# Kernel tuning notes

Hardware: AMD Instinct MI355X
Metric: run time of the kernel (lower is better)

The kernel has to match this reference:

```python
import jax, jax.numpy as jnp
import numpy as np

NUM_HEADS = 12
D_MODEL = 768
D_K = D_MODEL // NUM_HEADS


def setup_inputs() -> dict:
    key = jax.random.key(0)
    k0, k1, k2, k3, k4 = jax.random.split(key, 5)
    B, S = 4, 2048
    scale = 1.0 / np.sqrt(D_MODEL)
    return {
        "x": jax.random.normal(k0, (B, S, D_MODEL), dtype=jnp.float32),
        "wq": jax.random.normal(k1, (D_MODEL, D_MODEL), dtype=jnp.float32) * scale,
        "wk": jax.random.normal(k2, (D_MODEL, D_MODEL), dtype=jnp.float32) * scale,
        "wv": jax.random.normal(k3, (D_MODEL, D_MODEL), dtype=jnp.float32) * scale,
        "wo": jax.random.normal(k4, (D_MODEL, D_MODEL), dtype=jnp.float32) * scale,
    }


def reference(x, wq, wk, wv, wo):
    # x: [B, S, d_model]; weights are torch Linear weights [out, in], applied as x @ W^T
    B, S, _ = x.shape
    q = (x @ wq.T).reshape(B, S, NUM_HEADS, D_K).transpose(0, 2, 1, 3)  # [B,H,S,dk]
    k = (x @ wk.T).reshape(B, S, NUM_HEADS, D_K).transpose(0, 2, 1, 3)
    v = (x @ wv.T).reshape(B, S, NUM_HEADS, D_K).transpose(0, 2, 1, 3)
    # Note: original calls scaled_dot_product_attention(queries, keys, values),
    # whose body computes (first_arg @ second_arg^T) => standard Q K^T scores.
    scores = jnp.einsum("bhqd,bhkd->bhqk", q, k) / jnp.sqrt(jnp.float32(D_K))
    causal_mask = jnp.triu(jnp.ones((S, S), dtype=bool), k=1)  # True above diagonal
    scores = jnp.where(causal_mask, -jnp.inf, scores)
    probs = jax.nn.softmax(scores, axis=-1)  # stable max-subtracted softmax, as in source
    attn = jnp.einsum("bhqk,bhkd->bhqd", probs, v)  # [B,H,S,dk]
    attn = attn.transpose(0, 2, 1, 3).reshape(B, S, D_MODEL)
    return attn @ wo.T
```

## Files before the change

### kernel.cpp

```cpp
#include <hip/hip_runtime.h>
#include <stdint.h>

#define DMODEL 768
#define NHEADS 12
#define DK 64
#define BATCH 4
#define SEQ 2048
#define MTOK (BATCH*SEQ)

typedef float f32x4 __attribute__((ext_vector_type(4)));
typedef float f32x16 __attribute__((ext_vector_type(16)));
typedef short bf16x8 __attribute__((ext_vector_type(8)));
typedef unsigned short u16;
typedef unsigned int u32;

#define LOG2E 1.4426950408889634f

__device__ __forceinline__ u16 f2bf(float f) {
  uint32_t u = __float_as_uint(f);
  u += 0x7FFFu + ((u >> 16) & 1u);
  return (u16)(u >> 16);
}

#define GLDS16(g, l) __builtin_amdgcn_global_load_lds( \
    (const __attribute__((address_space(1))) unsigned int*)(g), \
    (__attribute__((address_space(3))) unsigned int*)(l), 16, 0, 0)

__global__ void cvt_kernel(const float* __restrict__ src, u16* __restrict__ dst, int n4) {
  int i = blockIdx.x * blockDim.x + threadIdx.x;
  if (i >= n4) return;
  float4 v = reinterpret_cast<const float4*>(src)[i];
  ushort4 o;
  o.x = f2bf(v.x); o.y = f2bf(v.y); o.z = f2bf(v.z); o.w = f2bf(v.w);
  reinterpret_cast<ushort4*>(dst)[i] = o;
}

__global__ void cvt_w4(const float* __restrict__ w0, const float* __restrict__ w1,
                       const float* __restrict__ w2, const float* __restrict__ w3,
                       u16* __restrict__ dst, int n4) {
  int i = blockIdx.x * blockDim.x + threadIdx.x;
  if (i >= n4) return;
  const float* src = (blockIdx.y == 0) ? w0 : (blockIdx.y == 1) ? w1 : (blockIdx.y == 2) ? w2 : w3;
  float4 v = reinterpret_cast<const float4*>(src)[i];
  ushort4 o;
  o.x = f2bf(v.x); o.y = f2bf(v.y); o.z = f2bf(v.z); o.w = f2bf(v.w);
  reinterpret_cast<ushort4*>(dst + (size_t)blockIdx.y * DMODEL * DMODEL)[i] = o;
}

#define BM 128
#define BN 128
#define BK 32

__device__ __forceinline__ void gemm_loop(const u16* __restrict__ A, const u16* __restrict__ W,
                                          int bm, int bn, int t, u16* As, u16* Ws,
                                          f32x4 (&acc)[4][4]) {
  const int lane = t & 63;
  const int wave = t >> 6;
  const int r16 = lane & 15, g = lane >> 4;
  const int wr = (wave >> 1) * 64;
  const int wc = (wave & 1) * 64;
  const int c0 = t, c1 = t + 256;
  const int r0 = c0 >> 2, k0 = ((c0 & 3) ^ ((c0 >> 3) & 3)) * 8;
  const int r1 = c1 >> 2, k1 = ((c1 & 3) ^ ((c1 >> 3) & 3)) * 8;
  const size_t a0 = (size_t)(bm + r0) * DMODEL + k0;
  const size_t a1 = (size_t)(bm + r1) * DMODEL + k1;
  const size_t w0 = (size_t)(bn + r0) * DMODEL + k0;
  const size_t w1 = (size_t)(bn + r1) * DMODEL + k1;

  GLDS16(A + a0, As + c0 * 8); GLDS16(A + a1, As + c1 * 8);
  GLDS16(W + w0, Ws + c0 * 8); GLDS16(W + w1, Ws + c1 * 8);
  __syncthreads();

  const int NK = DMODEL / BK;
  for (int kt = 0; kt < NK; ++kt) {
    const int cur = kt & 1;
    if (kt + 1 < NK) {
      const size_t koff = (size_t)(kt + 1) * BK;
      GLDS16(A + a0 + koff, As + (cur ^ 1) * 4096 + c0 * 8);
      GLDS16(A + a1 + koff, As + (cur ^ 1) * 4096 + c1 * 8);
      GLDS16(W + w0 + koff, Ws + (cur ^ 1) * 4096 + c0 * 8);
      GLDS16(W + w1 + koff, Ws + (cur ^ 1) * 4096 + c1 * 8);
    }
    bf16x8 af[4], bfr[4];
#pragma unroll
    for (int m = 0; m < 4; ++m) {
      const int row = wr + m * 16 + r16;
      af[m] = *reinterpret_cast<const bf16x8*>(&As[cur * 4096 + row * 32 + ((g ^ ((row >> 1) & 3)) * 8)]);
    }
#pragma unroll
    for (int n = 0; n < 4; ++n) {
      const int row = wc + n * 16 + r16;
      bfr[n] = *reinterpret_cast<const bf16x8*>(&Ws[cur * 4096 + row * 32 + ((g ^ ((row >> 1) & 3)) * 8)]);
    }
#pragma unroll
    for (int m = 0; m < 4; ++m)
#pragma unroll
      for (int n = 0; n < 4; ++n)
        acc[m][n] = __builtin_amdgcn_mfma_f32_16x16x32_bf16(af[m], bfr[n], acc[m][n], 0, 0, 0);
    __syncthreads();
  }
}

__launch_bounds__(256)
__global__ void qkv_gemm(const u16* __restrict__ A, const u16* __restrict__ wAll,
                         u16* __restrict__ Qw, u16* __restrict__ Kw, u16* __restrict__ Vtw) {
  __shared__ __align__(16) u16 As[2 * BM * BK];
  __shared__ __align__(16) u16 Ws[2 * BN * BK];
  const int t = threadIdx.x;
  const int lane = t & 63, wave = t >> 6;
  const int r16 = lane & 15, g = lane >> 4;
  const int bm = blockIdx.x * BM, bn = blockIdx.y * BN;
  const int z = blockIdx.z;
  const u16* W = wAll + (size_t)z * DMODEL * DMODEL;
  const int wr = (wave >> 1) * 64, wc = (wave & 1) * 64;

  f32x4 acc[4][4] = {};
  gemm_loop(A, W, bm, bn, t, As, Ws, acc);

  if (z <= 1) {
    u16* Qo = (z == 0) ? Qw : Kw;
    const float scl = (z == 0) ? (0.125f * LOG2E) : 1.0f;
#pragma unroll
    for (int m = 0; m < 4; ++m) {
      const int gi0 = bm + wr + m * 16 + g * 4;
#pragma unroll
      for (int n = 0; n < 4; ++n) {
        const int gj = bn + wc + n * 16 + r16;
        const int h = gj >> 6, dc = gj & 63;
#pragma unroll
        for (int r = 0; r < 4; ++r) {
          const int gi = gi0 + r;
          const int b_ = gi >> 11, s = gi & 2047;
          Qo[((size_t)((b_ * NHEADS + h) * SEQ + s) << 6) + dc] = f2bf(acc[m][n][r] * scl);
        }
      }
    }
  } else {
#pragma unroll
    for (int m = 0; m < 4; ++m) {
      const int gi0 = bm + wr + m * 16 + g * 4;
      const int b_ = gi0 >> 11, s0 = gi0 & 2047;
#pragma unroll
      for (int n = 0; n < 4; ++n) {
        const int gj = bn + wc + n * 16 + r16;
        const int h = gj >> 6, dc = gj & 63;
        ushort4 pk;
        pk.x = f2bf(acc[m][n][0]); pk.y = f2bf(acc[m][n][1]);
        pk.z = f2bf(acc[m][n][2]); pk.w = f2bf(acc[m][n][3]);
        *reinterpret_cast<ushort4*>(Vtw + ((size_t)((b_ * NHEADS + h) * DK + dc) * SEQ + s0)) = pk;
      }
    }
  }
}

__launch_bounds__(256)
__global__ void out_gemm(const u16* __restrict__ A, const u16* __restrict__ W,
                         float* __restrict__ C) {
  __shared__ __align__(16) u16 As[2 * BM * BK];
  __shared__ __align__(16) u16 Ws[2 * BN * BK];
  const int t = threadIdx.x;
  const int lane = t & 63, wave = t >> 6;
  const int r16 = lane & 15, g = lane >> 4;
  const int bm = blockIdx.x * BM, bn = blockIdx.y * BN;
  const int wr = (wave >> 1) * 64, wc = (wave & 1) * 64;

  f32x4 acc[4][4] = {};
  gemm_loop(A, W, bm, bn, t, As, Ws, acc);

#pragma unroll
  for (int m = 0; m < 4; ++m) {
    const int gi0 = bm + wr + m * 16 + g * 4;
#pragma unroll
    for (int n = 0; n < 4; ++n) {
      const int gj = bn + wc + n * 16 + r16;
#pragma unroll
      for (int r = 0; r < 4; ++r)
        C[(size_t)(gi0 + r) * DMODEL + gj] = acc[m][n][r];
    }
  }
}

__device__ __forceinline__ bf16x8 mk_pa(int hi, float p0, float p1, float p2, float p3,
                                        float p4, float p5, float p6, float p7) {
  u32 w01, w23, w45, w67;
  asm("v_cvt_pk_bf16_f32 %0, %1, %2" : "=v"(w01) : "v"(p0), "v"(p1));
  asm("v_cvt_pk_bf16_f32 %0, %1, %2" : "=v"(w23) : "v"(p2), "v"(p3));
  asm("v_cvt_pk_bf16_f32 %0, %1, %2" : "=v"(w45) : "v"(p4), "v"(p5));
  asm("v_cvt_pk_bf16_f32 %0, %1, %2" : "=v"(w67) : "v"(p6), "v"(p7));
  const u32 pw01 = (u32)__shfl_xor((int)w01, 32);
  const u32 pw23 = (u32)__shfl_xor((int)w23, 32);
  const u32 pw45 = (u32)__shfl_xor((int)w45, 32);
  const u32 pw67 = (u32)__shfl_xor((int)w67, 32);
  union { u32 w[4]; bf16x8 v; } u;
  u.w[0] = hi ? pw45 : w01;
  u.w[1] = hi ? pw67 : w23;
  u.w[2] = hi ? w45  : pw01;
  u.w[3] = hi ? w67  : pw23;
  return u.v;
}

__launch_bounds__(256, 2)
__global__ void attn_kernel(const u16* __restrict__ Qg, const u16* __restrict__ Kg,
                            const u16* __restrict__ Vtg, u16* __restrict__ Og) {
  __shared__ __align__(16) u16 Ks[2][64 * 64];
  __shared__ __align__(16) u16 Vs[2][64 * 64];
  const int t = threadIdx.x;
  const int lane = t & 63, warp = t >> 6;
  const int l31 = lane & 31, hi = lane >> 5;
  const int bx = blockIdx.x;
  const int qt = 15 - (bx / 48);
  const int hb = bx % 48;
  const int h = hb % NHEADS, b = hb / NHEADS;
  const int q0w = qt * 128 + warp * 32;
  const int nt = 2 * qt + 2;
  const size_t bh = (size_t)(b * NHEADS + h);
  const u16* Qb = Qg + bh * SEQ * DK;
  const u16* Kb = Kg + bh * SEQ * DK;
  const u16* Vb = Vtg + bh * DK * SEQ;

  int srow[2], scol[2];
#pragma unroll
  for (int j = 0; j < 2; ++j) {
    const int bb = (t + j * 256) * 16;
    srow[j] = bb >> 7;
    scol[j] = ((bb & 127) ^ ((srow[j] & 7) << 4)) >> 1;
  }

  const int q = q0w + l31;
  bf16x8 qf[4];
#pragma unroll
  for (int kk = 0; kk < 4; ++kk)
    qf[kk] = *reinterpret_cast<const bf16x8*>(Qb + (size_t)q * DK + kk * 16 + hi * 8);

  f32x16 o0 = {}, o1 = {};
  float m = -__builtin_inff(), l = 0.f;
  const int hi4 = hi * 4;
  const int xr = (l31 & 7) << 4;

#pragma unroll
  for (int j = 0; j < 2; ++j) {
    GLDS16(Kb + (size_t)srow[j] * DK + scol[j], &Ks[0][0] + (t + j * 256) * 8);
    GLDS16(Vb + (size_t)srow[j] * SEQ + scol[j], &Vs[0][0] + (t + j * 256) * 8);
  }
  __syncthreads();

  for (int i = 0; i < nt; ++i) {
    const int cur = i & 1;
    const int kv0 = i * 64;
    if (i + 1 < nt) {
      const int nkv0 = kv0 + 64;
#pragma unroll
      for (int j = 0; j < 2; ++j) {
        GLDS16(Kb + (size_t)(nkv0 + srow[j]) * DK + scol[j], &Ks[cur ^ 1][0] + (t + j * 256) * 8);
        GLDS16(Vb + (size_t)srow[j] * SEQ + nkv0 + scol[j], &Vs[cur ^ 1][0] + (t + j * 256) * 8);
      }
    }

    if (kv0 <= q0w + 31) {
      f32x16 t0 = {}, t1 = {};
      const char* Kc = (const char*)Ks[cur];
      __builtin_amdgcn_s_setprio(1);
#pragma unroll
      for (int kk = 0; kk < 4; ++kk) {
        const int cb = kk * 32 + hi * 16;
        bf16x8 a0 = *reinterpret_cast<const bf16x8*>(Kc + ((l31 * 128 + cb) ^ xr));
        bf16x8 a1 = *reinterpret_cast<const bf16x8*>(Kc + (((l31 + 32) * 128 + cb) ^ xr));
        t0 = __builtin_amdgcn_mfma_f32_32x32x16_bf16(a0, qf[kk], t0, 0, 0, 0);
        t1 = __builtin_amdgcn_mfma_f32_32x32x16_bf16(a1, qf[kk], t1, 0, 0, 0);
      }
      __builtin_amdgcn_s_setprio(0);

      if (kv0 + 63 > q0w) {
        const int qmh = (q - kv0) - hi4;
#pragma unroll
        for (int r = 0; r < 16; ++r) {
          const int kvc = (r & 3) + 8 * (r >> 2);
          if (kvc > qmh)      t0[r] = -__builtin_inff();
          if (kvc + 32 > qmh) t1[r] = -__builtin_inff();
        }
      }

      float x0 = fmaxf(t0[0], t0[1]),  x1 = fmaxf(t0[2], t0[3]);
      float x2 = fmaxf(t0[4], t0[5]),  x3 = fmaxf(t0[6], t0[7]);
      float x4 = fmaxf(t0[8], t0[9]),  x5 = fmaxf(t0[10], t0[11]);
      float x6 = fmaxf(t0[12], t0[13]), x7 = fmaxf(t0[14], t0[15]);
      x0 = fmaxf(x0, x1); x2 = fmaxf(x2, x3); x4 = fmaxf(x4, x5); x6 = fmaxf(x6, x7);
      float y0 = fmaxf(t1[0], t1[1]),  y1 = fmaxf(t1[2], t1[3]);
      float y2 = fmaxf(t1[4], t1[5]),  y3 = fmaxf(t1[6], t1[7]);
      float y4 = fmaxf(t1[8], t1[9]),  y5 = fmaxf(t1[10], t1[11]);
      float y6 = fmaxf(t1[12], t1[13]), y7 = fmaxf(t1[14], t1[15]);
      y0 = fmaxf(y0, y1); y2 = fmaxf(y2, y3); y4 = fmaxf(y4, y5); y6 = fmaxf(y6, y7);
      float pm = fmaxf(fmaxf(fmaxf(x0, x2), fmaxf(x4, x6)),
                       fmaxf(fmaxf(y0, y2), fmaxf(y4, y6)));
      pm = fmaxf(pm, __shfl_xor(pm, 32));

      if (pm > m) {
        const float corr = __builtin_amdgcn_exp2f(m - pm);
        l *= corr;
        o0 = o0 * corr;
        o1 = o1 * corr;
        m = pm;
      }

#pragma unroll
      for (int r = 0; r < 16; ++r) { t0[r] = __builtin_amdgcn_exp2f(t0[r] - m); }
#pragma unroll
      for (int r = 0; r < 16; ++r) { t1[r] = __builtin_amdgcn_exp2f(t1[r] - m); }
      float s0 = 0.f, s1 = 0.f, s2 = 0.f, s3 = 0.f;
#pragma unroll
      for (int r = 0; r < 4; ++r) {
        s0 += t0[r]; s1 += t0[4 + r]; s2 += t0[8 + r]; s3 += t0[12 + r];
        s0 += t1[r]; s1 += t1[4 + r]; s2 += t1[8 + r]; s3 += t1[12 + r];
      }
      float s = (s0 + s1) + (s2 + s3);
      l += s + __shfl_xor(s, 32);

      bf16x8 pa0 = mk_pa(hi, t0[0], t0[1], t0[2], t0[3], t0[4], t0[5], t0[6], t0[7]);
      bf16x8 pa1 = mk_pa(hi, t0[8], t0[9], t0[10], t0[11], t0[12], t0[13], t0[14], t0[15]);
      bf16x8 pa2 = mk_pa(hi, t1[0], t1[1], t1[2], t1[3], t1[4], t1[5], t1[6], t1[7]);
      bf16x8 pa3 = mk_pa(hi, t1[8], t1[9], t1[10], t1[11], t1[12], t1[13], t1[14], t1[15]);

      const char* Vc = (const char*)Vs[cur];
      __builtin_amdgcn_s_setprio(1);
#pragma unroll
      for (int ks = 0; ks < 4; ++ks) {
        const int cb = ks * 32 + hi * 16;
        bf16x8 v0 = *reinterpret_cast<const bf16x8*>(Vc + ((l31 * 128 + cb) ^ xr));
        bf16x8 v1 = *reinterpret_cast<const bf16x8*>(Vc + (((l31 + 32) * 128 + cb) ^ xr));
        const bf16x8 pk = (ks == 0) ? pa0 : (ks == 1) ? pa1 : (ks == 2) ? pa2 : pa3;
        o0 = __builtin_amdgcn_mfma_f32_32x32x16_bf16(v0, pk, o0, 0, 0, 0);
        o1 = __builtin_amdgcn_mfma_f32_32x32x16_bf16(v1, pk, o1, 0, 0, 0);
      }
      __builtin_amdgcn_s_setprio(0);
    }
    __syncthreads();
  }

  const float rinv = 1.0f / l;
  u16* orow = Og + (size_t)(b * SEQ + q) * DMODEL + h * 64;
#pragma unroll
  for (int j = 0; j < 4; ++j) {
    ushort4 pk;
    pk.x = f2bf(o0[4 * j + 0] * rinv); pk.y = f2bf(o0[4 * j + 1] * rinv);
    pk.z = f2bf(o0[4 * j + 2] * rinv); pk.w = f2bf(o0[4 * j + 3] * rinv);
    *reinterpret_cast<ushort4*>(orow + 8 * j + hi4) = pk;
  }
#pragma unroll
  for (int j = 0; j < 4; ++j) {
    ushort4 pk;
    pk.x = f2bf(o1[4 * j + 0] * rinv); pk.y = f2bf(o1[4 * j + 1] * rinv);
    pk.z = f2bf(o1[4 * j + 2] * rinv); pk.w = f2bf(o1[4 * j + 3] * rinv);
    *reinterpret_cast<ushort4*>(orow + 32 + 8 * j + hi4) = pk;
  }
}

extern "C" void kernel_launch(void* const* d_in, const int* in_sizes, int n_in,
                              void* d_out, int out_size, void* d_ws, size_t ws_size,
                              hipStream_t stream) {
  const float* x  = (const float*)d_in[0];
  const float* wq = (const float*)d_in[1];
  const float* wk = (const float*)d_in[2];
  const float* wv = (const float*)d_in[3];
  const float* wo = (const float*)d_in[4];

  const size_t SZ_TOK = (size_t)MTOK * DMODEL * 2;
  const size_t SZ_W   = (size_t)DMODEL * DMODEL * 2;
  char* ws = (char*)d_ws;
  size_t off = 0;
  u16* xb  = (u16*)(ws + off); off += SZ_TOK;
  u16* wqb = (u16*)(ws + off); off += 4 * SZ_W;
  u16* Qw  = (u16*)(ws + off); off += SZ_TOK;
  u16* Kw  = (u16*)(ws + off); off += SZ_TOK;
  u16* Vtw = (u16*)(ws + off); off += SZ_TOK;
  u16* Ow  = (u16*)(ws + off); off += SZ_TOK;
  if (ws_size < off) return;
  u16* wob = wqb + 3 * (size_t)DMODEL * DMODEL;

  const int nx4 = MTOK * DMODEL / 4;
  const int nw4 = DMODEL * DMODEL / 4;
  cvt_kernel<<<nx4 / 256, 256, 0, stream>>>(x, xb, nx4);
  cvt_w4<<<dim3(nw4 / 256, 4), 256, 0, stream>>>(wq, wk, wv, wo, wqb, nw4);

  qkv_gemm<<<dim3(MTOK / BM, DMODEL / BN, 3), 256, 0, stream>>>(xb, wqb, Qw, Kw, Vtw);

  attn_kernel<<<dim3(768), 256, 0, stream>>>(Qw, Kw, Vtw, Ow);

  out_gemm<<<dim3(MTOK / BM, DMODEL / BN), 256, 0, stream>>>(Ow, wob, (float*)d_out);
}
```

Measured before the change: 211.3 us.

## Merge conversion kernels, halve attention and out-GEMM tiles for more blocks

```diff
diff --git a/kernel.cpp b/kernel.cpp
--- a/kernel.cpp
+++ b/kernel.cpp
@@ -26,25 +26,27 @@
     (const __attribute__((address_space(1))) unsigned int*)(g), \
     (__attribute__((address_space(3))) unsigned int*)(l), 16, 0, 0)
 
-__global__ void cvt_kernel(const float* __restrict__ src, u16* __restrict__ dst, int n4) {
+__global__ void cvt_all(const float* __restrict__ x,
+                        const float* __restrict__ wq, const float* __restrict__ wk,
+                        const float* __restrict__ wv, const float* __restrict__ wo,
+                        u16* __restrict__ xb, u16* __restrict__ wb) {
+  const int NX = MTOK * DMODEL / 4;
+  const int NW = DMODEL * DMODEL / 4;
   int i = blockIdx.x * blockDim.x + threadIdx.x;
-  if (i >= n4) return;
-  float4 v = reinterpret_cast<const float4*>(src)[i];
+  const float* src; u16* dst; int idx;
+  if (i < NX) {
+    src = x; dst = xb; idx = i;
+  } else {
+    const int j = i - NX;
+    const int w = j / NW;
+    idx = j - w * NW;
+    src = (w == 0) ? wq : (w == 1) ? wk : (w == 2) ? wv : wo;
+    dst = wb + (size_t)w * DMODEL * DMODEL;
+  }
+  float4 v = reinterpret_cast<const float4*>(src)[idx];
   ushort4 o;
   o.x = f2bf(v.x); o.y = f2bf(v.y); o.z = f2bf(v.z); o.w = f2bf(v.w);
-  reinterpret_cast<ushort4*>(dst)[i] = o;
-}
-
-__global__ void cvt_w4(const float* __restrict__ w0, const float* __restrict__ w1,
-                       const float* __restrict__ w2, const float* __restrict__ w3,
-                       u16* __restrict__ dst, int n4) {
-  int i = blockIdx.x * blockDim.x + threadIdx.x;
-  if (i >= n4) return;
-  const float* src = (blockIdx.y == 0) ? w0 : (blockIdx.y == 1) ? w1 : (blockIdx.y == 2) ? w2 : w3;
-  float4 v = reinterpret_cast<const float4*>(src)[i];
-  ushort4 o;
-  o.x = f2bf(v.x); o.y = f2bf(v.y); o.z = f2bf(v.z); o.w = f2bf(v.w);
-  reinterpret_cast<ushort4*>(dst + (size_t)blockIdx.y * DMODEL * DMODEL)[i] = o;
+  reinterpret_cast<ushort4*>(dst)[idx] = o;
 }
 
 #define BM 128
@@ -156,19 +158,56 @@
 __launch_bounds__(256)
 __global__ void out_gemm(const u16* __restrict__ A, const u16* __restrict__ W,
                          float* __restrict__ C) {
-  __shared__ __align__(16) u16 As[2 * BM * BK];
+  __shared__ __align__(16) u16 As[2 * 64 * BK];
   __shared__ __align__(16) u16 Ws[2 * BN * BK];
   const int t = threadIdx.x;
   const int lane = t & 63, wave = t >> 6;
   const int r16 = lane & 15, g = lane >> 4;
-  const int bm = blockIdx.x * BM, bn = blockIdx.y * BN;
-  const int wr = (wave >> 1) * 64, wc = (wave & 1) * 64;
-
-  f32x4 acc[4][4] = {};
-  gemm_loop(A, W, bm, bn, t, As, Ws, acc);
-
-#pragma unroll
-  for (int m = 0; m < 4; ++m) {
+  const int bm = blockIdx.x * 64, bn = blockIdx.y * BN;
+  const int wr = (wave >> 1) * 32, wc = (wave & 1) * 64;
+
+  const int ca = t, ra = ca >> 2, ka = ((ca & 3) ^ ((ca >> 3) & 3)) * 8;
+  const int c1 = t + 256, r1 = c1 >> 2, k1 = ((c1 & 3) ^ ((c1 >> 3) & 3)) * 8;
+  const size_t aoff = (size_t)(bm + ra) * DMODEL + ka;
+  const size_t w0 = (size_t)(bn + ra) * DMODEL + ka;
+  const size_t w1 = (size_t)(bn + r1) * DMODEL + k1;
+
+  f32x4 acc[2][4] = {};
+
+  GLDS16(A + aoff, As + ca * 8);
+  GLDS16(W + w0, Ws + ca * 8); GLDS16(W + w1, Ws + c1 * 8);
+  __syncthreads();
+
+  const int NK = DMODEL / BK;
+  for (int kt = 0; kt < NK; ++kt) {
+    const int cur = kt & 1;
+    if (kt + 1 < NK) {
+      const size_t koff = (size_t)(kt + 1) * BK;
+      GLDS16(A + aoff + koff, As + (cur ^ 1) * 2048 + ca * 8);
+      GLDS16(W + w0 + koff, Ws + (cur ^ 1) * 4096 + ca * 8);
+      GLDS16(W + w1 + koff, Ws + (cur ^ 1) * 4096 + c1 * 8);
+    }
+    bf16x8 af[2], bfr[4];
+#pragma unroll
+    for (int m = 0; m < 2; ++m) {
+      const int row = wr + m * 16 + r16;
+      af[m] = *reinterpret_cast<const bf16x8*>(&As[cur * 2048 + row * 32 + ((g ^ ((row >> 1) & 3)) * 8)]);
+    }
+#pragma unroll
+    for (int n = 0; n < 4; ++n) {
+      const int row = wc + n * 16 + r16;
+      bfr[n] = *reinterpret_cast<const bf16x8*>(&Ws[cur * 4096 + row * 32 + ((g ^ ((row >> 1) & 3)) * 8)]);
+    }
+#pragma unroll
+    for (int m = 0; m < 2; ++m)
+#pragma unroll
+      for (int n = 0; n < 4; ++n)
+        acc[m][n] = __builtin_amdgcn_mfma_f32_16x16x32_bf16(af[m], bfr[n], acc[m][n], 0, 0, 0);
+    __syncthreads();
+  }
+
+#pragma unroll
+  for (int m = 0; m < 2; ++m) {
     const int gi0 = bm + wr + m * 16 + g * 4;
 #pragma unroll
     for (int n = 0; n < 4; ++n) {
@@ -199,7 +238,7 @@
   return u.v;
 }
 
-__launch_bounds__(256, 2)
+__launch_bounds__(128)
 __global__ void attn_kernel(const u16* __restrict__ Qg, const u16* __restrict__ Kg,
                             const u16* __restrict__ Vtg, u16* __restrict__ Og) {
   __shared__ __align__(16) u16 Ks[2][64 * 64];
@@ -208,20 +247,20 @@
   const int lane = t & 63, warp = t >> 6;
   const int l31 = lane & 31, hi = lane >> 5;
   const int bx = blockIdx.x;
-  const int qt = 15 - (bx / 48);
+  const int qt = 31 - (bx / 48);
   const int hb = bx % 48;
   const int h = hb % NHEADS, b = hb / NHEADS;
-  const int q0w = qt * 128 + warp * 32;
-  const int nt = 2 * qt + 2;
+  const int q0w = qt * 64 + warp * 32;
+  const int nt = qt + 1;
   const size_t bh = (size_t)(b * NHEADS + h);
   const u16* Qb = Qg + bh * SEQ * DK;
   const u16* Kb = Kg + bh * SEQ * DK;
   const u16* Vb = Vtg + bh * DK * SEQ;
 
-  int srow[2], scol[2];
-#pragma unroll
-  for (int j = 0; j < 2; ++j) {
-    const int bb = (t + j * 256) * 16;
+  int srow[4], scol[4];
+#pragma unroll
+  for (int j = 0; j < 4; ++j) {
+    const int bb = (t + j * 128) * 16;
     srow[j] = bb >> 7;
     scol[j] = ((bb & 127) ^ ((srow[j] & 7) << 4)) >> 1;
   }
@@ -238,9 +277,9 @@
   const int xr = (l31 & 7) << 4;
 
 #pragma unroll
-  for (int j = 0; j < 2; ++j) {
-    GLDS16(Kb + (size_t)srow[j] * DK + scol[j], &Ks[0][0] + (t + j * 256) * 8);
-    GLDS16(Vb + (size_t)srow[j] * SEQ + scol[j], &Vs[0][0] + (t + j * 256) * 8);
+  for (int j = 0; j < 4; ++j) {
+    GLDS16(Kb + (size_t)srow[j] * DK + scol[j], &Ks[0][0] + (t + j * 128) * 8);
+    GLDS16(Vb + (size_t)srow[j] * SEQ + scol[j], &Vs[0][0] + (t + j * 128) * 8);
   }
   __syncthreads();
 
@@ -250,13 +289,13 @@
     if (i + 1 < nt) {
       const int nkv0 = kv0 + 64;
 #pragma unroll
-      for (int j = 0; j < 2; ++j) {
-        GLDS16(Kb + (size_t)(nkv0 + srow[j]) * DK + scol[j], &Ks[cur ^ 1][0] + (t + j * 256) * 8);
-        GLDS16(Vb + (size_t)srow[j] * SEQ + nkv0 + scol[j], &Vs[cur ^ 1][0] + (t + j * 256) * 8);
-      }
-    }
-
-    if (kv0 <= q0w + 31) {
+      for (int j = 0; j < 4; ++j) {
+        GLDS16(Kb + (size_t)(nkv0 + srow[j]) * DK + scol[j], &Ks[cur ^ 1][0] + (t + j * 128) * 8);
+        GLDS16(Vb + (size_t)srow[j] * SEQ + nkv0 + scol[j], &Vs[cur ^ 1][0] + (t + j * 128) * 8);
+      }
+    }
+
+    {
       f32x16 t0 = {}, t1 = {};
       const char* Kc = (const char*)Ks[cur];
       __builtin_amdgcn_s_setprio(1);
@@ -376,14 +415,13 @@
   if (ws_size < off) return;
   u16* wob = wqb + 3 * (size_t)DMODEL * DMODEL;
 
-  const int nx4 = MTOK * DMODEL / 4;
-  const int nw4 = DMODEL * DMODEL / 4;
-  cvt_kernel<<<nx4 / 256, 256, 0, stream>>>(x, xb, nx4);
-  cvt_w4<<<dim3(nw4 / 256, 4), 256, 0, stream>>>(wq, wk, wv, wo, wqb, nw4);
+  const int NX = MTOK * DMODEL / 4;
+  const int NW = DMODEL * DMODEL / 4;
+  cvt_all<<<(NX + 4 * NW) / 256, 256, 0, stream>>>(x, wq, wk, wv, wo, xb, wqb);
 
   qkv_gemm<<<dim3(MTOK / BM, DMODEL / BN, 3), 256, 0, stream>>>(xb, wqb, Qw, Kw, Vtw);
 
-  attn_kernel<<<dim3(768), 256, 0, stream>>>(Qw, Kw, Vtw, Ow);
-
-  out_gemm<<<dim3(MTOK / BM, DMODEL / BN), 256, 0, stream>>>(Ow, wob, (float*)d_out);
-}
+  attn_kernel<<<dim3(1536), 128, 0, stream>>>(Qw, Kw, Vtw, Ow);
+
+  out_gemm<<<dim3(MTOK / 64, DMODEL / BN), 256, 0, stream>>>(Ow, wob, (float*)d_out);
+}
```

Result: no change. 215.4 us (+1.9%).
